# Kernel tuning notes

Hardware: AMD Instinct MI355X
Metric: run time of the kernel (lower is better)

## Reference

```python
import jax, jax.numpy as jnp
import numpy as np

B, H, S, D = 2, 16, 4096, 64
WIN = 512
HALF = WIN // 2  # stride of the sliding window


def setup_inputs() -> dict:
    key = jax.random.key(0)
    kq, kk, kv = jax.random.split(key, 3)
    Q = jax.random.normal(kq, (B, H, S, D), dtype=jnp.float32)
    K = jax.random.normal(kk, (B, H, S, D), dtype=jnp.float32)
    V = jax.random.normal(kv, (B, H, S, D), dtype=jnp.float32)
    scale = jnp.float32(1.0 / np.sqrt(D))
    return {"Q": Q, "K": K, "V": V, "scale": scale}


def _window_attn(Q, K, V, scale):
    # sigmoid attention normalized to sum 1 over keys (use_sigmoid=True path)
    scores = jnp.einsum('...qd,...kd->...qk', Q, K) * scale
    attn = jax.nn.sigmoid(scores)
    attn = attn / jnp.sum(attn, axis=-1, keepdims=True)
    return jnp.einsum('...qk,...kd->...qd', attn, V)


def reference(Q, K, V, scale):
    b, h, s, d = Q.shape
    n_full = (s - WIN) // HALF + 1
    starts = jnp.arange(n_full) * HALF
    idx = starts[:, None] + jnp.arange(WIN)
    Qw = Q[:, :, idx, :]
    Kw = K[:, :, idx, :]
    Vw = V[:, :, idx, :]
    out_w = _window_attn(Qw, Kw, Vw, scale)

    # trailing partial window of length HALF starting at n_full*HALF
    p0 = n_full * HALF
    out_p = _window_attn(Q[:, :, p0:, :], K[:, :, p0:, :], V[:, :, p0:, :], scale)  # [b,h,HALF,d]

    alpha = jnp.linspace(0.0, 1.0, HALF, dtype=Q.dtype).reshape(1, 1, HALF, 1)
    fh = out_w[:, :, :, :HALF, :]   # first halves of each full window
    sh = out_w[:, :, :, HALF:, :]   # second halves

    a5 = alpha[:, :, None]          # [1,1,1,HALF,1]
    # overlap blend: region starting at w*HALF (w>=1) mixes window w-1's 2nd half
    # with window w's 1st half
    mid = (1 - a5) * sh[:, :, :-1] + a5 * fh[:, :, 1:]     # [b,h,n_full-1,HALF,d]
    mid = mid.reshape(b, h, (n_full - 1) * HALF, d)
    tail = (1 - alpha) * sh[:, :, -1] + alpha * out_p       # [b,h,HALF,d]
    return jnp.concatenate([fh[:, :, 0], mid, tail], axis=2)
```

## Files before the change

### kernel.cpp

```cpp
#include <hip/hip_runtime.h>
#include <stdint.h>

#define NB 2
#define NH 16
#define SEQ 4096
#define DD 64
#define NM 16
#define QB 256
#define CH 256
#define VSTR 528

typedef __attribute__((ext_vector_type(8)))  __bf16 bf16x8;
typedef __attribute__((ext_vector_type(16))) float  f32x16;
typedef __attribute__((ext_vector_type(2)))  unsigned int u32x2;

static __device__ __forceinline__ f32x16 zero16() {
    f32x16 z;
#pragma unroll
    for (int i = 0; i < 16; i++) z[i] = 0.0f;
    return z;
}

__global__ void __launch_bounds__(256)
cvt_k_kernel(const float* __restrict__ K, __bf16* __restrict__ kw)
{
    const size_t gid = (size_t)blockIdx.x * 256 + threadIdx.x;
    const float* src = K + gid * 16;
    float4 a = *(const float4*)(src);
    float4 b = *(const float4*)(src + 4);
    float4 c = *(const float4*)(src + 8);
    float4 d = *(const float4*)(src + 12);
    bf16x8 o0, o1;
    o0[0] = (__bf16)a.x; o0[1] = (__bf16)a.y; o0[2] = (__bf16)a.z; o0[3] = (__bf16)a.w;
    o0[4] = (__bf16)b.x; o0[5] = (__bf16)b.y; o0[6] = (__bf16)b.z; o0[7] = (__bf16)b.w;
    o1[0] = (__bf16)c.x; o1[1] = (__bf16)c.y; o1[2] = (__bf16)c.z; o1[3] = (__bf16)c.w;
    o1[4] = (__bf16)d.x; o1[5] = (__bf16)d.y; o1[6] = (__bf16)d.z; o1[7] = (__bf16)d.w;
    *(bf16x8*)(kw + gid * 16)     = o0;
    *(bf16x8*)(kw + gid * 16 + 8) = o1;
}

template<bool PRE>
__global__ void __launch_bounds__(512, 2)
swa_kernel(const float* __restrict__ Q, const float* __restrict__ K,
           const float* __restrict__ V, const float* __restrict__ scale_p,
           const __bf16* __restrict__ kw, float* __restrict__ out)
{
    int lid = (int)blockIdx.x;
    lid = (lid & 7) * 64 + (lid >> 3);
    const int m  = lid & 15;
    const int bh = lid >> 4;

    const float scale = scale_p[0];
    const float* Qb = Q + (size_t)bh * SEQ * DD;
    const float* Kb = K + (size_t)bh * SEQ * DD;
    const float* Vb = V + (size_t)bh * SEQ * DD;
    const __bf16* kwb = kw + (size_t)bh * SEQ * DD;
    float*       Ob = out + (size_t)bh * SEQ * DD;

    const int tid  = threadIdx.x;
    const int lane = tid & 63;
    const int w    = tid >> 6;
    const int l31  = lane & 31;
    const int h5   = lane >> 5;

    __shared__ __align__(16) unsigned char vt[64 * VSTR];

    bf16x8 qf[4];
    {
        const float* qp = Qb + (size_t)(m * QB + w * 32 + l31) * DD + 8 * h5;
#pragma unroll
        for (int s = 0; s < 4; s++) {
            float4 a = *(const float4*)(qp + 16 * s);
            float4 b = *(const float4*)(qp + 16 * s + 4);
            bf16x8 f;
            f[0] = (__bf16)(a.x * scale); f[1] = (__bf16)(a.y * scale);
            f[2] = (__bf16)(a.z * scale); f[3] = (__bf16)(a.w * scale);
            f[4] = (__bf16)(b.x * scale); f[5] = (__bf16)(b.y * scale);
            f[6] = (__bf16)(b.z * scale); f[7] = (__bf16)(b.w * scale);
            qf[s] = f;
        }
    }

    f32x16 accA0 = zero16(), accA1 = zero16();
    f32x16 accB0 = zero16(), accB1 = zero16();
    float dA = 0.0f, dB = 0.0f;

    for (int ci = 0; ci < 3; ci++) {
        const int ck = (m - 1 + ci) * CH;
        if (ck < 0 || ck >= SEQ) continue;
        const bool inA = (m > 0) && (ci <= 1);
        const bool inB = (ci >= 1);

        __syncthreads();
        {
            const int kk = (tid & 127) * 2;
            const int dg = tid >> 7;
            const float* vp0 = Vb + (size_t)(ck + kk) * DD + dg * 16;
            const float* vp1 = vp0 + DD;
#pragma unroll
            for (int j = 0; j < 16; j += 4) {
                float4 a = *(const float4*)(vp0 + j);
                float4 b = *(const float4*)(vp1 + j);
                float av[4] = {a.x, a.y, a.z, a.w};
                float bv[4] = {b.x, b.y, b.z, b.w};
#pragma unroll
                for (int e = 0; e < 4; e++) {
                    union { __bf16 h[2]; uint32_t u; } pk;
                    pk.h[0] = (__bf16)av[e];
                    pk.h[1] = (__bf16)bv[e];
                    *(uint32_t*)(vt + (size_t)(dg * 16 + j + e) * VSTR + kk * 2) = pk.u;
                }
            }
        }

        bf16x8 kcur[4];
        if (PRE) {
            const __bf16* p = kwb + (size_t)(ck + l31) * DD + 8 * h5;
#pragma unroll
            for (int s = 0; s < 4; s++) kcur[s] = *(const bf16x8*)(p + 16 * s);
        }
        __syncthreads();

#pragma unroll 2
        for (int kt = 0; kt < 8; kt++) {
            f32x16 st = zero16();
            bf16x8 knx[4];
            if (PRE) {
                if (kt < 7) {
                    const __bf16* p = kwb + (size_t)(ck + (kt + 1) * 32 + l31) * DD + 8 * h5;
#pragma unroll
                    for (int s = 0; s < 4; s++) knx[s] = *(const bf16x8*)(p + 16 * s);
                }
#pragma unroll
                for (int s = 0; s < 4; s++)
                    st = __builtin_amdgcn_mfma_f32_32x32x16_bf16(kcur[s], qf[s], st, 0, 0, 0);
            } else {
                const float* kp = Kb + (size_t)(ck + kt * 32 + l31) * DD + 8 * h5;
#pragma unroll
                for (int s = 0; s < 4; s++) {
                    float4 a = *(const float4*)(kp + 16 * s);
                    float4 b = *(const float4*)(kp + 16 * s + 4);
                    bf16x8 f;
                    f[0] = (__bf16)a.x; f[1] = (__bf16)a.y; f[2] = (__bf16)a.z; f[3] = (__bf16)a.w;
                    f[4] = (__bf16)b.x; f[5] = (__bf16)b.y; f[6] = (__bf16)b.z; f[7] = (__bf16)b.w;
                    st = __builtin_amdgcn_mfma_f32_32x32x16_bf16(f, qf[s], st, 0, 0, 0);
                }
            }

            uint32_t wv[8];
            float dsum = 0.0f;
#pragma unroll
            for (int i = 0; i < 8; i++) {
                float p0 = __builtin_amdgcn_rcpf(1.0f + __expf(-st[2 * i]));
                float p1 = __builtin_amdgcn_rcpf(1.0f + __expf(-st[2 * i + 1]));
                dsum += p0 + p1;
                union { __bf16 h[2]; uint32_t u; } pk;
                pk.h[0] = (__bf16)p0;
                pk.h[1] = (__bf16)p1;
                wv[i] = pk.u;
            }
            if (inA) dA += dsum;
            if (inB) dB += dsum;

            u32x2 rA = __builtin_amdgcn_permlane32_swap(wv[0], wv[2], false, false);
            u32x2 rB = __builtin_amdgcn_permlane32_swap(wv[1], wv[3], false, false);
            u32x2 rC = __builtin_amdgcn_permlane32_swap(wv[4], wv[6], false, false);
            u32x2 rD = __builtin_amdgcn_permlane32_swap(wv[5], wv[7], false, false);
            union { uint32_t u[4]; bf16x8 v; } A0, A1;
            A0.u[0] = rA[0]; A0.u[1] = rB[0]; A0.u[2] = rA[1]; A0.u[3] = rB[1];
            A1.u[0] = rC[0]; A1.u[1] = rD[0]; A1.u[2] = rC[1]; A1.u[3] = rD[1];

            const unsigned char* vrow0 = vt + (size_t)l31 * VSTR;
            const unsigned char* vrow1 = vt + (size_t)(32 + l31) * VSTR;
            const int ko = kt * 64 + h5 * 16;
            bf16x8 v00 = *(const bf16x8*)(vrow0 + ko);
            bf16x8 v01 = *(const bf16x8*)(vrow0 + ko + 32);
            bf16x8 v10 = *(const bf16x8*)(vrow1 + ko);
            bf16x8 v11 = *(const bf16x8*)(vrow1 + ko + 32);

            if (inA) {
                accA0 = __builtin_amdgcn_mfma_f32_32x32x16_bf16(A0.v, v00, accA0, 0, 0, 0);
                accA0 = __builtin_amdgcn_mfma_f32_32x32x16_bf16(A1.v, v01, accA0, 0, 0, 0);
                accA1 = __builtin_amdgcn_mfma_f32_32x32x16_bf16(A0.v, v10, accA1, 0, 0, 0);
                accA1 = __builtin_amdgcn_mfma_f32_32x32x16_bf16(A1.v, v11, accA1, 0, 0, 0);
            }
            if (inB) {
                accB0 = __builtin_amdgcn_mfma_f32_32x32x16_bf16(A0.v, v00, accB0, 0, 0, 0);
                accB0 = __builtin_amdgcn_mfma_f32_32x32x16_bf16(A1.v, v01, accB0, 0, 0, 0);
                accB1 = __builtin_amdgcn_mfma_f32_32x32x16_bf16(A0.v, v10, accB1, 0, 0, 0);
                accB1 = __builtin_amdgcn_mfma_f32_32x32x16_bf16(A1.v, v11, accB1, 0, 0, 0);
            }
            if (PRE) {
#pragma unroll
                for (int s = 0; s < 4; s++) kcur[s] = knx[s];
            }
        }
    }

    const float dAt = dA + __shfl_xor(dA, 32, 64);
    const float dBt = dB + __shfl_xor(dB, 32, 64);
    const float invA = __builtin_amdgcn_rcpf(dAt);
    const float invB = __builtin_amdgcn_rcpf(dBt);

#pragma unroll
    for (int r = 0; r < 16; r++) {
        const int cr = (r & 3) + 8 * (r >> 2) + 4 * h5;
        const int j  = w * 32 + cr;
        const float ia = __shfl(invA, cr, 64);
        const float ib = __shfl(invB, cr, 64);
        float o0, o1;
        if (m == 0) {
            o0 = accB0[r] * ib;
            o1 = accB1[r] * ib;
        } else {
            const float alpha = (float)j * (1.0f / 255.0f);
            o0 = (1.0f - alpha) * (accA0[r] * ia) + alpha * (accB0[r] * ib);
            o1 = (1.0f - alpha) * (accA1[r] * ia) + alpha * (accB1[r] * ib);
        }
        float* orow = Ob + (size_t)(m * QB + j) * DD;
        orow[l31]      = o0;
        orow[32 + l31] = o1;
    }
}

extern "C" void kernel_launch(void* const* d_in, const int* in_sizes, int n_in,
                              void* d_out, int out_size, void* d_ws, size_t ws_size,
                              hipStream_t stream) {
    const float* Q = (const float*)d_in[0];
    const float* K = (const float*)d_in[1];
    const float* V = (const float*)d_in[2];
    const float* s = (const float*)d_in[3];
    float* out = (float*)d_out;

    const size_t kElems  = (size_t)NB * NH * SEQ * DD;
    const size_t kBytes  = kElems * sizeof(__bf16);
    dim3 grid(NB * NH * NM, 1, 1);
    dim3 block(512, 1, 1);

    if (ws_size >= kBytes) {
        __bf16* kw = (__bf16*)d_ws;
        dim3 cg((unsigned)(kElems / 16 / 256), 1, 1);
        hipLaunchKernelGGL(cvt_k_kernel, cg, dim3(256, 1, 1), 0, stream, K, kw);
        hipLaunchKernelGGL((swa_kernel<true>), grid, block, 0, stream, Q, K, V, s, kw, out);
    } else {
        hipLaunchKernelGGL((swa_kernel<false>), grid, block, 0, stream, Q, K, V, s,
                           (const __bf16*)nullptr, out);
    }
}
```

Baseline: 193.5 us.

## Pre-tile K and transpose V to bf16, stream 64-key tiles through double-buffered LDS

K is now written to workspace as bf16 in an MFMA-fragment tiled layout, and V is pre-transposed to bf16 64-key tiles by a new conversion kernel. The main kernel copies one contiguous 8KB K tile and one V tile per step into double-buffered shared memory, prefetching the next tile into registers. This is meant to replace strided global K loads and the in-kernel fp32 V transpose with coalesced 16-byte loads and less conversion work inside the attention kernel. The cost is an extra kernel launch, an extra pass over V, and more workspace use. It also adds a barrier every 64 keys instead of every 256.

```diff
diff --git a/kernel.cpp b/kernel.cpp
--- a/kernel.cpp
+++ b/kernel.cpp
@@ -9,6 +9,7 @@
 #define QB 256
 #define CH 256
 #define VSTR 528
+#define VTS 144
 
 typedef __attribute__((ext_vector_type(8)))  __bf16 bf16x8;
 typedef __attribute__((ext_vector_type(16))) float  f32x16;
@@ -22,10 +23,12 @@
 }
 
 __global__ void __launch_bounds__(256)
-cvt_k_kernel(const float* __restrict__ K, __bf16* __restrict__ kw)
+cvt_k_kernel(const float* __restrict__ K, unsigned char* __restrict__ kw)
 {
-    const size_t gid = (size_t)blockIdx.x * 256 + threadIdx.x;
-    const float* src = K + gid * 16;
+    const int t   = blockIdx.x * 256 + threadIdx.x;
+    const int g   = t >> 2;
+    const int sdp = t & 3;
+    const float* src = K + (size_t)g * DD + sdp * 16;
     float4 a = *(const float4*)(src);
     float4 b = *(const float4*)(src + 4);
     float4 c = *(const float4*)(src + 8);
@@ -35,15 +38,45 @@
     o0[4] = (__bf16)b.x; o0[5] = (__bf16)b.y; o0[6] = (__bf16)b.z; o0[7] = (__bf16)b.w;
     o1[0] = (__bf16)c.x; o1[1] = (__bf16)c.y; o1[2] = (__bf16)c.z; o1[3] = (__bf16)c.w;
     o1[4] = (__bf16)d.x; o1[5] = (__bf16)d.y; o1[6] = (__bf16)d.z; o1[7] = (__bf16)d.w;
-    *(bf16x8*)(kw + gid * 16)     = o0;
-    *(bf16x8*)(kw + gid * 16 + 8) = o1;
-}
-
-template<bool PRE>
+    const int sub = (g >> 5) & 1, k31 = g & 31;
+    unsigned char* db = kw + (size_t)(g >> 6) * 8192 + (sub * 4 + sdp) * 1024;
+    *(bf16x8*)(db + k31 * 16)        = o0;
+    *(bf16x8*)(db + (k31 + 32) * 16) = o1;
+}
+
+__global__ void __launch_bounds__(256)
+cvt_v_kernel(const float* __restrict__ V, unsigned char* __restrict__ vw)
+{
+    __shared__ __align__(16) unsigned char vt[64 * VTS];
+    const int tile = blockIdx.x;
+    const int t    = threadIdx.x;
+    const int kk   = t >> 2;
+    const int sdp  = t & 3;
+    const float* src = V + ((size_t)tile * 64 + kk) * DD + sdp * 16;
+#pragma unroll
+    for (int j = 0; j < 4; j++) {
+        float4 f = *(const float4*)(src + 4 * j);
+        float fv[4] = {f.x, f.y, f.z, f.w};
+#pragma unroll
+        for (int e = 0; e < 4; e++) {
+            const int d = sdp * 16 + 4 * j + e;
+            *(__bf16*)(vt + d * VTS + kk * 2) = (__bf16)fv[e];
+        }
+    }
+    __syncthreads();
+#pragma unroll
+    for (int p = 0; p < 2; p++) {
+        const int idx = p * 4096 + t * 16;
+        const int d = idx >> 7, cb = idx & 127;
+        bf16x8 r = *(const bf16x8*)(vt + d * VTS + cb);
+        *(bf16x8*)(vw + (size_t)tile * 8192 + idx) = r;
+    }
+}
+
 __global__ void __launch_bounds__(512, 2)
-swa_kernel(const float* __restrict__ Q, const float* __restrict__ K,
-           const float* __restrict__ V, const float* __restrict__ scale_p,
-           const __bf16* __restrict__ kw, float* __restrict__ out)
+swa_pre_kernel(const float* __restrict__ Q, const float* __restrict__ scale_p,
+               const unsigned char* __restrict__ kw, const unsigned char* __restrict__ vw,
+               float* __restrict__ out)
 {
     int lid = (int)blockIdx.x;
     lid = (lid & 7) * 64 + (lid >> 3);
@@ -52,10 +85,9 @@
 
     const float scale = scale_p[0];
     const float* Qb = Q + (size_t)bh * SEQ * DD;
-    const float* Kb = K + (size_t)bh * SEQ * DD;
-    const float* Vb = V + (size_t)bh * SEQ * DD;
-    const __bf16* kwb = kw + (size_t)bh * SEQ * DD;
-    float*       Ob = out + (size_t)bh * SEQ * DD;
+    const unsigned char* kwb = kw + (size_t)bh * (SEQ / 64) * 8192;
+    const unsigned char* vwb = vw + (size_t)bh * (SEQ / 64) * 8192;
+    float* Ob = out + (size_t)bh * SEQ * DD;
 
     const int tid  = threadIdx.x;
     const int lane = tid & 63;
@@ -63,7 +95,8 @@
     const int l31  = lane & 31;
     const int h5   = lane >> 5;
 
-    __shared__ __align__(16) unsigned char vt[64 * VSTR];
+    __shared__ __align__(16) unsigned char kbuf[2][8192];
+    __shared__ __align__(16) unsigned char vbuf[2][64 * VTS];
 
     bf16x8 qf[4];
     {
@@ -85,66 +118,44 @@
     f32x16 accB0 = zero16(), accB1 = zero16();
     float dA = 0.0f, dB = 0.0f;
 
-    for (int ci = 0; ci < 3; ci++) {
-        const int ck = (m - 1 + ci) * CH;
-        if (ck < 0 || ck >= SEQ) continue;
-        const bool inA = (m > 0) && (ci <= 1);
-        const bool inB = (ci >= 1);
+    const int c0 = (m > 0) ? m - 1 : 0;
+    const int c1 = (m < 15) ? m + 1 : 15;
+    const int T  = (c1 - c0 + 1) * 4;
+
+    const int vdst = tid * 16 + (tid >> 3) * 16;
+
+    bf16x8 g0, g1;
+    {
+        const size_t tb = (size_t)(c0 * 4) * 8192 + tid * 16;
+        g0 = *(const bf16x8*)(kwb + tb);
+        g1 = *(const bf16x8*)(vwb + tb);
+    }
+
+    for (int ti = 0; ti < T; ++ti) {
+        const int c = c0 + (ti >> 2);
+        const bool inA = (m > 0) && (c <= m);
+        const bool inB = (c >= m);
+        unsigned char* kb = kbuf[ti & 1];
+        unsigned char* vb = vbuf[ti & 1];
 
         __syncthreads();
-        {
-            const int kk = (tid & 127) * 2;
-            const int dg = tid >> 7;
-            const float* vp0 = Vb + (size_t)(ck + kk) * DD + dg * 16;
-            const float* vp1 = vp0 + DD;
-#pragma unroll
-            for (int j = 0; j < 16; j += 4) {
-                float4 a = *(const float4*)(vp0 + j);
-                float4 b = *(const float4*)(vp1 + j);
-                float av[4] = {a.x, a.y, a.z, a.w};
-                float bv[4] = {b.x, b.y, b.z, b.w};
-#pragma unroll
-                for (int e = 0; e < 4; e++) {
-                    union { __bf16 h[2]; uint32_t u; } pk;
-                    pk.h[0] = (__bf16)av[e];
-                    pk.h[1] = (__bf16)bv[e];
-                    *(uint32_t*)(vt + (size_t)(dg * 16 + j + e) * VSTR + kk * 2) = pk.u;
-                }
-            }
-        }
-
-        bf16x8 kcur[4];
-        if (PRE) {
-            const __bf16* p = kwb + (size_t)(ck + l31) * DD + 8 * h5;
-#pragma unroll
-            for (int s = 0; s < 4; s++) kcur[s] = *(const bf16x8*)(p + 16 * s);
+        *(bf16x8*)(kb + tid * 16) = g0;
+        *(bf16x8*)(vb + vdst)     = g1;
+        if (ti + 1 < T) {
+            const size_t tb = (size_t)((c0 + ((ti + 1) >> 2)) * 4 + ((ti + 1) & 3)) * 8192
+                              + tid * 16;
+            g0 = *(const bf16x8*)(kwb + tb);
+            g1 = *(const bf16x8*)(vwb + tb);
         }
         __syncthreads();
 
-#pragma unroll 2
-        for (int kt = 0; kt < 8; kt++) {
+#pragma unroll
+        for (int kt = 0; kt < 2; ++kt) {
             f32x16 st = zero16();
-            bf16x8 knx[4];
-            if (PRE) {
-                if (kt < 7) {
-                    const __bf16* p = kwb + (size_t)(ck + (kt + 1) * 32 + l31) * DD + 8 * h5;
-#pragma unroll
-                    for (int s = 0; s < 4; s++) knx[s] = *(const bf16x8*)(p + 16 * s);
-                }
-#pragma unroll
-                for (int s = 0; s < 4; s++)
-                    st = __builtin_amdgcn_mfma_f32_32x32x16_bf16(kcur[s], qf[s], st, 0, 0, 0);
-            } else {
-                const float* kp = Kb + (size_t)(ck + kt * 32 + l31) * DD + 8 * h5;
-#pragma unroll
-                for (int s = 0; s < 4; s++) {
-                    float4 a = *(const float4*)(kp + 16 * s);
-                    float4 b = *(const float4*)(kp + 16 * s + 4);
-                    bf16x8 f;
-                    f[0] = (__bf16)a.x; f[1] = (__bf16)a.y; f[2] = (__bf16)a.z; f[3] = (__bf16)a.w;
-                    f[4] = (__bf16)b.x; f[5] = (__bf16)b.y; f[6] = (__bf16)b.z; f[7] = (__bf16)b.w;
-                    st = __builtin_amdgcn_mfma_f32_32x32x16_bf16(f, qf[s], st, 0, 0, 0);
-                }
+#pragma unroll
+            for (int s = 0; s < 4; s++) {
+                bf16x8 kf = *(const bf16x8*)(kb + (kt * 4 + s) * 1024 + lane * 16);
+                st = __builtin_amdgcn_mfma_f32_32x32x16_bf16(kf, qf[s], st, 0, 0, 0);
             }
 
             uint32_t wv[8];
@@ -170,13 +181,11 @@
             A0.u[0] = rA[0]; A0.u[1] = rB[0]; A0.u[2] = rA[1]; A0.u[3] = rB[1];
             A1.u[0] = rC[0]; A1.u[1] = rD[0]; A1.u[2] = rC[1]; A1.u[3] = rD[1];
 
-            const unsigned char* vrow0 = vt + (size_t)l31 * VSTR;
-            const unsigned char* vrow1 = vt + (size_t)(32 + l31) * VSTR;
             const int ko = kt * 64 + h5 * 16;
-            bf16x8 v00 = *(const bf16x8*)(vrow0 + ko);
-            bf16x8 v01 = *(const bf16x8*)(vrow0 + ko + 32);
-            bf16x8 v10 = *(const bf16x8*)(vrow1 + ko);
-            bf16x8 v11 = *(const bf16x8*)(vrow1 + ko + 32);
+            bf16x8 v00 = *(const bf16x8*)(vb + l31 * VTS + ko);
+            bf16x8 v01 = *(const bf16x8*)(vb + l31 * VTS + ko + 32);
+            bf16x8 v10 = *(const bf16x8*)(vb + (32 + l31) * VTS + ko);
+            bf16x8 v11 = *(const bf16x8*)(vb + (32 + l31) * VTS + ko + 32);
 
             if (inA) {
                 accA0 = __builtin_amdgcn_mfma_f32_32x32x16_bf16(A0.v, v00, accA0, 0, 0, 0);
@@ -189,10 +198,6 @@
                 accB0 = __builtin_amdgcn_mfma_f32_32x32x16_bf16(A1.v, v01, accB0, 0, 0, 0);
                 accB1 = __builtin_amdgcn_mfma_f32_32x32x16_bf16(A0.v, v10, accB1, 0, 0, 0);
                 accB1 = __builtin_amdgcn_mfma_f32_32x32x16_bf16(A1.v, v11, accB1, 0, 0, 0);
-            }
-            if (PRE) {
-#pragma unroll
-                for (int s = 0; s < 4; s++) kcur[s] = knx[s];
             }
         }
     }
@@ -223,6 +228,164 @@
     }
 }
 
+__global__ void __launch_bounds__(512, 2)
+swa_fb_kernel(const float* __restrict__ Q, const float* __restrict__ K,
+              const float* __restrict__ V, const float* __restrict__ scale_p,
+              float* __restrict__ out)
+{
+    int lid = (int)blockIdx.x;
+    lid = (lid & 7) * 64 + (lid >> 3);
+    const int m  = lid & 15;
+    const int bh = lid >> 4;
+
+    const float scale = scale_p[0];
+    const float* Qb = Q + (size_t)bh * SEQ * DD;
+    const float* Kb = K + (size_t)bh * SEQ * DD;
+    const float* Vb = V + (size_t)bh * SEQ * DD;
+    float*       Ob = out + (size_t)bh * SEQ * DD;
+
+    const int tid  = threadIdx.x;
+    const int lane = tid & 63;
+    const int w    = tid >> 6;
+    const int l31  = lane & 31;
+    const int h5   = lane >> 5;
+
+    __shared__ __align__(16) unsigned char vt[64 * VSTR];
+
+    bf16x8 qf[4];
+    {
+        const float* qp = Qb + (size_t)(m * QB + w * 32 + l31) * DD + 8 * h5;
+#pragma unroll
+        for (int s = 0; s < 4; s++) {
+            float4 a = *(const float4*)(qp + 16 * s);
+            float4 b = *(const float4*)(qp + 16 * s + 4);
+            bf16x8 f;
+            f[0] = (__bf16)(a.x * scale); f[1] = (__bf16)(a.y * scale);
+            f[2] = (__bf16)(a.z * scale); f[3] = (__bf16)(a.w * scale);
+            f[4] = (__bf16)(b.x * scale); f[5] = (__bf16)(b.y * scale);
+            f[6] = (__bf16)(b.z * scale); f[7] = (__bf16)(b.w * scale);
+            qf[s] = f;
+        }
+    }
+
+    f32x16 accA0 = zero16(), accA1 = zero16();
+    f32x16 accB0 = zero16(), accB1 = zero16();
+    float dA = 0.0f, dB = 0.0f;
+
+    for (int ci = 0; ci < 3; ci++) {
+        const int ck = (m - 1 + ci) * CH;
+        if (ck < 0 || ck >= SEQ) continue;
+        const bool inA = (m > 0) && (ci <= 1);
+        const bool inB = (ci >= 1);
+
+        __syncthreads();
+        {
+            const int kk = (tid & 127) * 2;
+            const int dg = tid >> 7;
+            const float* vp0 = Vb + (size_t)(ck + kk) * DD + dg * 16;
+            const float* vp1 = vp0 + DD;
+#pragma unroll
+            for (int j = 0; j < 16; j += 4) {
+                float4 a = *(const float4*)(vp0 + j);
+                float4 b = *(const float4*)(vp1 + j);
+                float av[4] = {a.x, a.y, a.z, a.w};
+                float bv[4] = {b.x, b.y, b.z, b.w};
+#pragma unroll
+                for (int e = 0; e < 4; e++) {
+                    union { __bf16 h[2]; uint32_t u; } pk;
+                    pk.h[0] = (__bf16)av[e];
+                    pk.h[1] = (__bf16)bv[e];
+                    *(uint32_t*)(vt + (size_t)(dg * 16 + j + e) * VSTR + kk * 2) = pk.u;
+                }
+            }
+        }
+        __syncthreads();
+
+        for (int kt = 0; kt < 8; kt++) {
+            const float* kp = Kb + (size_t)(ck + kt * 32 + l31) * DD + 8 * h5;
+            f32x16 st = zero16();
+#pragma unroll
+            for (int s = 0; s < 4; s++) {
+                float4 a = *(const float4*)(kp + 16 * s);
+                float4 b = *(const float4*)(kp + 16 * s + 4);
+                bf16x8 f;
+                f[0] = (__bf16)a.x; f[1] = (__bf16)a.y; f[2] = (__bf16)a.z; f[3] = (__bf16)a.w;
+                f[4] = (__bf16)b.x; f[5] = (__bf16)b.y; f[6] = (__bf16)b.z; f[7] = (__bf16)b.w;
+                st = __builtin_amdgcn_mfma_f32_32x32x16_bf16(f, qf[s], st, 0, 0, 0);
+            }
+
+            uint32_t wv[8];
+            float dsum = 0.0f;
+#pragma unroll
+            for (int i = 0; i < 8; i++) {
+                float p0 = __builtin_amdgcn_rcpf(1.0f + __expf(-st[2 * i]));
+                float p1 = __builtin_amdgcn_rcpf(1.0f + __expf(-st[2 * i + 1]));
+                dsum += p0 + p1;
+                union { __bf16 h[2]; uint32_t u; } pk;
+                pk.h[0] = (__bf16)p0;
+                pk.h[1] = (__bf16)p1;
+                wv[i] = pk.u;
+            }
+            if (inA) dA += dsum;
+            if (inB) dB += dsum;
+
+            u32x2 rA = __builtin_amdgcn_permlane32_swap(wv[0], wv[2], false, false);
+            u32x2 rB = __builtin_amdgcn_permlane32_swap(wv[1], wv[3], false, false);
+            u32x2 rC = __builtin_amdgcn_permlane32_swap(wv[4], wv[6], false, false);
+            u32x2 rD = __builtin_amdgcn_permlane32_swap(wv[5], wv[7], false, false);
+            union { uint32_t u[4]; bf16x8 v; } A0, A1;
+            A0.u[0] = rA[0]; A0.u[1] = rB[0]; A0.u[2] = rA[1]; A0.u[3] = rB[1];
+            A1.u[0] = rC[0]; A1.u[1] = rD[0]; A1.u[2] = rC[1]; A1.u[3] = rD[1];
+
+            const unsigned char* vrow0 = vt + (size_t)l31 * VSTR;
+            const unsigned char* vrow1 = vt + (size_t)(32 + l31) * VSTR;
+            const int ko = kt * 64 + h5 * 16;
+            bf16x8 v00 = *(const bf16x8*)(vrow0 + ko);
+            bf16x8 v01 = *(const bf16x8*)(vrow0 + ko + 32);
+            bf16x8 v10 = *(const bf16x8*)(vrow1 + ko);
+            bf16x8 v11 = *(const bf16x8*)(vrow1 + ko + 32);
+
+            if (inA) {
+                accA0 = __builtin_amdgcn_mfma_f32_32x32x16_bf16(A0.v, v00, accA0, 0, 0, 0);
+                accA0 = __builtin_amdgcn_mfma_f32_32x32x16_bf16(A1.v, v01, accA0, 0, 0, 0);
+                accA1 = __builtin_amdgcn_mfma_f32_32x32x16_bf16(A0.v, v10, accA1, 0, 0, 0);
+                accA1 = __builtin_amdgcn_mfma_f32_32x32x16_bf16(A1.v, v11, accA1, 0, 0, 0);
+            }
+            if (inB) {
+                accB0 = __builtin_amdgcn_mfma_f32_32x32x16_bf16(A0.v, v00, accB0, 0, 0, 0);
+                accB0 = __builtin_amdgcn_mfma_f32_32x32x16_bf16(A1.v, v01, accB0, 0, 0, 0);
+                accB1 = __builtin_amdgcn_mfma_f32_32x32x16_bf16(A0.v, v10, accB1, 0, 0, 0);
+                accB1 = __builtin_amdgcn_mfma_f32_32x32x16_bf16(A1.v, v11, accB1, 0, 0, 0);
+            }
+        }
+    }
+
+    const float dAt = dA + __shfl_xor(dA, 32, 64);
+    const float dBt = dB + __shfl_xor(dB, 32, 64);
+    const float invA = __builtin_amdgcn_rcpf(dAt);
+    const float invB = __builtin_amdgcn_rcpf(dBt);
+
+#pragma unroll
+    for (int r = 0; r < 16; r++) {
+        const int cr = (r & 3) + 8 * (r >> 2) + 4 * h5;
+        const int j  = w * 32 + cr;
+        const float ia = __shfl(invA, cr, 64);
+        const float ib = __shfl(invB, cr, 64);
+        float o0, o1;
+        if (m == 0) {
+            o0 = accB0[r] * ib;
+            o1 = accB1[r] * ib;
+        } else {
+            const float alpha = (float)j * (1.0f / 255.0f);
+            o0 = (1.0f - alpha) * (accA0[r] * ia) + alpha * (accB0[r] * ib);
+            o1 = (1.0f - alpha) * (accA1[r] * ia) + alpha * (accB1[r] * ib);
+        }
+        float* orow = Ob + (size_t)(m * QB + j) * DD;
+        orow[l31]      = o0;
+        orow[32 + l31] = o1;
+    }
+}
+
 extern "C" void kernel_launch(void* const* d_in, const int* in_sizes, int n_in,
                               void* d_out, int out_size, void* d_ws, size_t ws_size,
                               hipStream_t stream) {
@@ -232,18 +395,19 @@
     const float* s = (const float*)d_in[3];
     float* out = (float*)d_out;
 
-    const size_t kElems  = (size_t)NB * NH * SEQ * DD;
-    const size_t kBytes  = kElems * sizeof(__bf16);
+    const size_t halfBytes = (size_t)NB * NH * SEQ * DD * 2;
     dim3 grid(NB * NH * NM, 1, 1);
     dim3 block(512, 1, 1);
 
-    if (ws_size >= kBytes) {
-        __bf16* kw = (__bf16*)d_ws;
-        dim3 cg((unsigned)(kElems / 16 / 256), 1, 1);
-        hipLaunchKernelGGL(cvt_k_kernel, cg, dim3(256, 1, 1), 0, stream, K, kw);
-        hipLaunchKernelGGL((swa_kernel<true>), grid, block, 0, stream, Q, K, V, s, kw, out);
+    if (ws_size >= 2 * halfBytes) {
+        unsigned char* kw = (unsigned char*)d_ws;
+        unsigned char* vw = kw + halfBytes;
+        dim3 cgk((unsigned)((size_t)NB * NH * SEQ * 4 / 256), 1, 1);
+        dim3 cgv((unsigned)((size_t)NB * NH * SEQ / 64), 1, 1);
+        hipLaunchKernelGGL(cvt_k_kernel, cgk, dim3(256, 1, 1), 0, stream, K, kw);
+        hipLaunchKernelGGL(cvt_v_kernel, cgv, dim3(256, 1, 1), 0, stream, V, vw);
+        hipLaunchKernelGGL(swa_pre_kernel, grid, block, 0, stream, Q, s, kw, vw, out);
     } else {
-        hipLaunchKernelGGL((swa_kernel<false>), grid, block, 0, stream, Q, K, V, s,
-                           (const __bf16*)nullptr, out);
-    }
-}
+        hipLaunchKernelGGL(swa_fb_kernel, grid, block, 0, stream, Q, K, V, s, out);
+    }
+}
```

Result: faster. 184.1 us (-4.8%).
